# Performance work log

Hardware: AMD Instinct MI355X
Metric: run time of the kernel (lower is better)

The kernel has to match this reference:

```python
import jax, jax.numpy as jnp
import numpy as np

EPS_BN = 1e-5
EPS_LN = 1e-5
B_, CIN, COUT, H_, W_ = 8, 64, 128, 64, 64
DSTATE, DCONV, EXPAND = 16, 4, 2
DINNER = EXPAND * COUT            # 256
DTRANK = (COUT + 15) // 16        # 8


def setup_inputs() -> dict:
    key = jax.random.key(0)
    ks = jax.random.split(key, 24)
    g = lambda i, shape, s=0.02: jax.random.normal(ks[i], shape, jnp.float32) * s
    inp = {}
    inp["x"] = jax.random.normal(ks[0], (B_, CIN, H_, W_), jnp.float32)
    # conv-bn-relu x2
    inp["conv1_w"] = g(1, (COUT, CIN, 3, 3), 0.05)
    inp["conv1_b"] = jnp.zeros((COUT,), jnp.float32)
    inp["bn1_g"] = jnp.ones((COUT,), jnp.float32)
    inp["bn1_b"] = jnp.zeros((COUT,), jnp.float32)
    inp["bn1_m"] = g(2, (COUT,), 0.1)
    inp["bn1_v"] = jnp.ones((COUT,), jnp.float32)
    inp["conv2_w"] = g(3, (COUT, COUT, 3, 3), 0.05)
    inp["conv2_b"] = jnp.zeros((COUT,), jnp.float32)
    inp["bn2_g"] = jnp.ones((COUT,), jnp.float32)
    inp["bn2_b"] = jnp.zeros((COUT,), jnp.float32)
    inp["bn2_m"] = g(4, (COUT,), 0.1)
    inp["bn2_v"] = jnp.ones((COUT,), jnp.float32)
    # Mamba params (mamba_ssm defaults: projections bias-free except dt_proj)
    inp["in_proj_w"] = g(5, (2 * DINNER, COUT))
    inp["conv1d_w"] = g(6, (DINNER, 1, DCONV), 0.1)   # depthwise
    inp["conv1d_b"] = jnp.zeros((DINNER,), jnp.float32)
    inp["x_proj_w"] = g(7, (DTRANK + 2 * DSTATE, DINNER))
    inp["dt_proj_w"] = g(8, (DINNER, DTRANK), 0.1)
    inp["dt_proj_b"] = g(9, (DINNER,), 0.5)
    # S4D-real init: A = -[1..d_state] per channel
    A = jnp.tile(jnp.arange(1, DSTATE + 1, dtype=jnp.float32)[None, :], (DINNER, 1))
    inp["A_log"] = jnp.log(A)
    inp["D"] = jnp.ones((DINNER,), jnp.float32)
    inp["out_proj_w"] = g(10, (COUT, DINNER))
    inp["ln_g"] = jnp.ones((COUT,), jnp.float32)
    inp["ln_b"] = jnp.zeros((COUT,), jnp.float32)
    return inp


def _conv3x3(x, w, b):
    y = jax.lax.conv_general_dilated(x, w, (1, 1), ((1, 1), (1, 1)),
                                     dimension_numbers=("NCHW", "OIHW", "NCHW"))
    return y + b[None, :, None, None]


def _bn_eval(x, g, b, m, v):
    inv = jax.lax.rsqrt(v + EPS_BN)
    return (x - m[None, :, None, None]) * (g * inv)[None, :, None, None] + b[None, :, None, None]


def _mamba(x_flat, in_proj_w, conv1d_w, conv1d_b, x_proj_w, dt_proj_w, dt_proj_b, A_log, D, out_proj_w):
    # x_flat: (B, L, C)
    Bsz, L, _ = x_flat.shape
    xz = jnp.einsum("blc,ec->ble", x_flat, in_proj_w)          # (B, L, 2*di)
    xm, z = jnp.split(xz, 2, axis=-1)                           # each (B, L, di)
    # causal depthwise conv1d over time
    xt = jnp.transpose(xm, (0, 2, 1))                           # (B, di, L)
    xt = jax.lax.conv_general_dilated(xt, conv1d_w, (1,), ((DCONV - 1, 0),),
                                      dimension_numbers=("NCH", "OIH", "NCH"),
                                      feature_group_count=DINNER)
    xt = xt + conv1d_b[None, :, None]
    x_ssm = jax.nn.silu(jnp.transpose(xt, (0, 2, 1)))           # (B, L, di)
    xdb = jnp.einsum("bld,ed->ble", x_ssm, x_proj_w)            # (B, L, dt_rank+2*ds)
    dt_r = xdb[..., :DTRANK]
    Bm = xdb[..., DTRANK:DTRANK + DSTATE]                       # (B, L, ds)
    Cm = xdb[..., DTRANK + DSTATE:]                             # (B, L, ds)
    dt = jax.nn.softplus(jnp.einsum("blr,dr->bld", dt_r, dt_proj_w) + dt_proj_b)
    A = -jnp.exp(A_log)                                         # (di, ds)

    def step(h, inp):
        dt_t, B_t, C_t, x_t = inp                               # (B,di) (B,ds) (B,ds) (B,di)
        dA = jnp.exp(dt_t[:, :, None] * A)                      # (B, di, ds)
        h = dA * h + (dt_t * x_t)[:, :, None] * B_t[:, None, :]
        y = jnp.einsum("bds,bs->bd", h, C_t)
        return h, y

    xs = (jnp.swapaxes(dt, 0, 1), jnp.swapaxes(Bm, 0, 1),
          jnp.swapaxes(Cm, 0, 1), jnp.swapaxes(x_ssm, 0, 1))
    h0 = jnp.zeros((Bsz, DINNER, DSTATE), jnp.float32)
    _, ys = jax.lax.scan(step, h0, xs)                          # (L, B, di)
    y = jnp.swapaxes(ys, 0, 1) + D * x_ssm
    y = y * jax.nn.silu(z)
    return jnp.einsum("bld,od->blo", y, out_proj_w)             # (B, L, C)


def reference(x, conv1_w, conv1_b, bn1_g, bn1_b, bn1_m, bn1_v,
              conv2_w, conv2_b, bn2_g, bn2_b, bn2_m, bn2_v,
              in_proj_w, conv1d_w, conv1d_b, x_proj_w, dt_proj_w, dt_proj_b,
              A_log, D, out_proj_w, ln_g, ln_b):
    h = jax.nn.relu(_bn_eval(_conv3x3(x, conv1_w, conv1_b), bn1_g, bn1_b, bn1_m, bn1_v))
    h = jax.nn.relu(_bn_eval(_conv3x3(h, conv2_w, conv2_b), bn2_g, bn2_b, bn2_m, bn2_v))
    Bsz, C, Hh, Ww = h.shape
    seq = jnp.transpose(h, (0, 2, 3, 1)).reshape(Bsz, Hh * Ww, C)
    seq = _mamba(seq, in_proj_w, conv1d_w, conv1d_b, x_proj_w,
                 dt_proj_w, dt_proj_b, A_log, D, out_proj_w)
    # LayerNorm over channels
    mu = jnp.mean(seq, axis=-1, keepdims=True)
    var = jnp.mean(jnp.square(seq - mu), axis=-1, keepdims=True)
    seq = (seq - mu) * jax.lax.rsqrt(var + EPS_LN) * ln_g + ln_b
    return jnp.transpose(seq.reshape(Bsz, Hh, Ww, C), (0, 3, 1, 2))
```

## Files before the change

kernel.cpp:

```cpp
#include <hip/hip_runtime.h>
#include <hip/hip_bf16.h>


typedef __attribute__((ext_vector_type(8))) short bf16x8;
typedef __attribute__((ext_vector_type(4))) float f32x4;

#define DEV __device__ __forceinline__

constexpr float LOG2E = 1.44269504088896f;

DEV float siluf(float v) {
  return v * __builtin_amdgcn_rcpf(1.f + __expf(-v));
}

DEV unsigned short f2bf(float f) {
  __hip_bfloat16 h = __float2bfloat16(f);
  return *reinterpret_cast<unsigned short*>(&h);
}

DEV float bf2f(unsigned short u) {
  unsigned int x = (unsigned int)u << 16;
  return __builtin_bit_cast(float, x);
}

DEV void gll16(const void* g, void* l) {
  __builtin_amdgcn_global_load_lds(
      (const __attribute__((address_space(1))) void*)g,
      (__attribute__((address_space(3))) void*)l, 16, 0, 0);
}

constexpr int NC = 256;
constexpr int CL = 16;

__global__ __launch_bounds__(256) void nchw2nhwc_bf16(
    const float* __restrict__ X, unsigned short* __restrict__ Xb)
{
  __shared__ float t[64][65];
  const int by = blockIdx.x;
  const int b = by >> 6, y = by & 63;
  const int tid = threadIdx.x;
  for (int i = tid; i < 4096; i += 256) {
    int c = i >> 6, xx = i & 63;
    t[c][xx] = X[(((size_t)b * 64 + c) * 64 + y) * 64 + xx];
  }
  __syncthreads();
  for (int i = tid; i < 4096; i += 256) {
    int xx = i >> 6, c = i & 63;
    Xb[(((size_t)(b * 66 + y + 1) * 66) + xx + 1) * 64 + c] = f2bf(t[c][xx]);
  }
}

__global__ __launch_bounds__(256) void prep_all(
    const float* __restrict__ conv1_w, const float* __restrict__ conv2_w,
    const float* __restrict__ in_proj_w, const float* __restrict__ out_proj_w,
    const float* __restrict__ x_proj_w, const float* __restrict__ A_log,
    unsigned short* __restrict__ wb1, unsigned short* __restrict__ wb2,
    unsigned short* __restrict__ win, unsigned short* __restrict__ wout,
    unsigned short* __restrict__ xpwb, float* __restrict__ An2f)
{
  int idx = blockIdx.x * 256 + threadIdx.x;
  if (idx < 73728) {
    int co = idx / 576, r = idx % 576, t = r >> 6, ci = r & 63;
    wb1[idx] = f2bf(conv1_w[((size_t)co * 64 + ci) * 9 + t]);
  } else if (idx < 221184) {
    int i = idx - 73728;
    int co = i / 1152, r = i % 1152, t = r >> 7, ci = r & 127;
    wb2[i] = f2bf(conv2_w[((size_t)co * 128 + ci) * 9 + t]);
  } else if (idx < 286720) {
    int i = idx - 221184; win[i] = f2bf(in_proj_w[i]);
  } else if (idx < 319488) {
    int i = idx - 286720; wout[i] = f2bf(out_proj_w[i]);
  } else if (idx < 352256) {
    int i = idx - 319488; int r = i >> 8, c = i & 255;
    xpwb[i] = (r < 40) ? f2bf(x_proj_w[r * 256 + c]) : (unsigned short)0;
  } else if (idx < 356352) {
    int i = idx - 352256;
    An2f[i] = -__expf(A_log[i]) * LOG2E;
  }
}

template<int CI, int PADOUT>
__global__ __launch_bounds__(256) void conv_mfma(
    const unsigned short* __restrict__ Xp,
    const unsigned short* __restrict__ Wb,
    const float* __restrict__ bc,
    const float* __restrict__ bg, const float* __restrict__ bb,
    const float* __restrict__ bm, const float* __restrict__ bv,
    unsigned short* __restrict__ Y)
{
  constexpr int KC  = 3 * CI / 64;
  constexpr int NCH = 3 * KC;
  __shared__ bf16x8 ldsA[2][512];

  const int lane = threadIdx.x & 63;
  const int wid  = threadIdx.x >> 6;
  const int n0 = wid * 32;
  const int y = blockIdx.x, b = blockIdx.y;
  const int lr = lane & 15, kq = lane >> 4, lk = kq * 8;

  auto stage = [&](int buf, int c) {
    const int dy = c / KC, kc = c - dy * KC;
    const unsigned short* g = Xp
        + (size_t)((b * 66 + y + dy) * 66) * CI
        + (size_t)lane * CI + kc * 64 + wid * 16;
    gll16(g,     &ldsA[buf][(wid * 2) * 64]);
    gll16(g + 8, &ldsA[buf][(wid * 2 + 1) * 64]);
  };

  f32x4 acc[4][2];
  #pragma unroll
  for (int i = 0; i < 4; ++i)
    #pragma unroll
    for (int j = 0; j < 2; ++j) acc[i][j] = f32x4{0.f, 0.f, 0.f, 0.f};

  stage(0, 0);
  __syncthreads();

  #pragma unroll
  for (int c = 0; c < NCH; ++c) {
    if (c + 1 < NCH) stage((c + 1) & 1, c + 1);
    const int dy = c / KC, kc = c - dy * KC;
    bf16x8 bw[2][2];
    #pragma unroll
    for (int t = 0; t < 2; ++t)
      #pragma unroll
      for (int nf = 0; nf < 2; ++nf)
        bw[t][nf] = *reinterpret_cast<const bf16x8*>(
            Wb + (size_t)(n0 + nf * 16 + lr) * (9 * CI)
               + dy * 3 * CI + kc * 64 + t * 32 + lk);
    const bf16x8* Ab = ldsA[c & 1];
    #pragma unroll
    for (int t = 0; t < 2; ++t)
      #pragma unroll
      for (int mf = 0; mf < 4; ++mf) {
        bf16x8 afr = Ab[(t * 4 + kq) * 64 + mf * 16 + lr];
        #pragma unroll
        for (int nf = 0; nf < 2; ++nf)
          acc[mf][nf] = __builtin_amdgcn_mfma_f32_16x16x32_bf16(
              afr, bw[t][nf], acc[mf][nf], 0, 0, 0);
      }
    __syncthreads();
  }

  #pragma unroll
  for (int nf = 0; nf < 2; ++nf) {
    int n = n0 + nf * 16 + lr;
    float aS = bg[n] * rsqrtf(bv[n] + 1e-5f);
    float aB = (bc[n] - bm[n]) * aS + bb[n];
    #pragma unroll
    for (int mf = 0; mf < 4; ++mf)
      #pragma unroll
      for (int i = 0; i < 4; ++i) {
        int m = mf * 16 + kq * 4 + i;
        float v = fmaxf(acc[mf][nf][i] * aS + aB, 0.f);
        if (PADOUT)
          Y[((size_t)(b * 66 + y + 1) * 66 + m + 1) * 128 + n] = f2bf(v);
        else
          Y[((size_t)(b * 4096 + y * 64 + m)) * 128 + n] = f2bf(v);
      }
  }
}

template<int KDIM, int EPI>
__global__ __launch_bounds__(256) void gemm_mfma(
    const unsigned short* __restrict__ A,
    const unsigned short* __restrict__ Wn,
    float* __restrict__ C0,
    unsigned short* __restrict__ Cb0, unsigned short* __restrict__ Cb1)
{
  constexpr int NCH = KDIM / 64;
  __shared__ bf16x8 ldsA[2][512];

  const int lane = threadIdx.x & 63;
  const int wid  = threadIdx.x >> 6;
  const int m0 = blockIdx.x * 64;
  const int n0 = blockIdx.y * 128 + wid * 32;
  const int lr = lane & 15, kq = lane >> 4, lk = kq * 8;

  bf16x8 bw[NCH][2][2];
  #pragma unroll
  for (int c = 0; c < NCH; ++c)
    #pragma unroll
    for (int t = 0; t < 2; ++t)
      #pragma unroll
      for (int nf = 0; nf < 2; ++nf)
        bw[c][t][nf] = *reinterpret_cast<const bf16x8*>(
            Wn + (size_t)(n0 + nf * 16 + lr) * KDIM + c * 64 + t * 32 + lk);

  auto stage = [&](int buf, int c) {
    const unsigned short* g = A + (size_t)(m0 + lane) * KDIM + c * 64 + wid * 16;
    gll16(g,     &ldsA[buf][(wid * 2) * 64]);
    gll16(g + 8, &ldsA[buf][(wid * 2 + 1) * 64]);
  };

  f32x4 acc[4][2];
  #pragma unroll
  for (int i = 0; i < 4; ++i)
    #pragma unroll
    for (int j = 0; j < 2; ++j) acc[i][j] = f32x4{0.f, 0.f, 0.f, 0.f};

  stage(0, 0);
  __syncthreads();

  #pragma unroll
  for (int c = 0; c < NCH; ++c) {
    if (c + 1 < NCH) stage((c + 1) & 1, c + 1);
    const bf16x8* Ab = ldsA[c & 1];
    #pragma unroll
    for (int t = 0; t < 2; ++t)
      #pragma unroll
      for (int mf = 0; mf < 4; ++mf) {
        bf16x8 afr = Ab[(t * 4 + kq) * 64 + mf * 16 + lr];
        #pragma unroll
        for (int nf = 0; nf < 2; ++nf)
          acc[mf][nf] = __builtin_amdgcn_mfma_f32_16x16x32_bf16(
              afr, bw[c][t][nf], acc[mf][nf], 0, 0, 0);
      }
    __syncthreads();
  }

  #pragma unroll
  for (int nf = 0; nf < 2; ++nf) {
    int n = n0 + nf * 16 + lr;
    #pragma unroll
    for (int mf = 0; mf < 4; ++mf)
      #pragma unroll
      for (int i = 0; i < 4; ++i) {
        int m = m0 + mf * 16 + kq * 4 + i;
        float v = acc[mf][nf][i];
        if (EPI == 0) {
          if (n < 256) Cb0[(size_t)m * 256 + n] = f2bf(v);
          else         Cb1[(size_t)m * 256 + (n - 256)] = f2bf(v);
        } else if (EPI == 1) {
          C0[(size_t)m * 128 + n] = v;
        } else {
          if (n < 40) C0[(size_t)m * 40 + n] = v;
        }
      }
  }
}

__global__ __launch_bounds__(256) void conv1d_silu(
    const unsigned short* __restrict__ xm,
    const float* __restrict__ w,
    const float* __restrict__ bias,
    unsigned short* __restrict__ out)
{
  __shared__ float ws4[4][256];
  __shared__ float bsh[256];
  for (int i = threadIdx.x; i < 1024; i += 256)
    ws4[i >> 8][i & 255] = w[(i & 255) * 4 + (i >> 8)];
  bsh[threadIdx.x] = bias[threadIdx.x];
  __syncthreads();
  const int total = 32768 * 32;
  for (int idx = blockIdx.x * 256 + threadIdx.x; idx < total;
       idx += gridDim.x * 256) {
    int d8 = idx & 31, t = idx >> 5, l = t & 4095;
    int d = d8 * 8;
    float acc[8];
    #pragma unroll
    for (int k = 0; k < 8; ++k) acc[k] = bsh[d + k];
    #pragma unroll
    for (int j = 0; j < 4; ++j) {
      if (l - 3 + j >= 0) {
        uint4 xv = *reinterpret_cast<const uint4*>(
            &xm[(size_t)(t - 3 + j) * 256 + d]);
        const unsigned short* xs = reinterpret_cast<const unsigned short*>(&xv);
        #pragma unroll
        for (int k = 0; k < 8; ++k)
          acc[k] = fmaf(bf2f(xs[k]), ws4[j][d + k], acc[k]);
      }
    }
    unsigned int pk[4];
    #pragma unroll
    for (int k = 0; k < 4; ++k) {
      unsigned short lo = f2bf(siluf(acc[2 * k]));
      unsigned short hi = f2bf(siluf(acc[2 * k + 1]));
      pk[k] = (unsigned int)lo | ((unsigned int)hi << 16);
    }
    *reinterpret_cast<uint4*>(&out[(size_t)t * 256 + d]) =
        *reinterpret_cast<uint4*>(pk);
  }
}

__global__ __launch_bounds__(256) void scan_pass1(
    const unsigned short* __restrict__ xssm, const float* __restrict__ xdb,
    const float* __restrict__ dtw, const float* __restrict__ dtb,
    const float* __restrict__ An2f,
    unsigned short* __restrict__ Qb, float* __restrict__ S)
{
  __shared__ __align__(16) float sh[CL][40];
  const int c = blockIdx.x, b = blockIdx.y;
  const int d = threadIdx.x;
  if (threadIdx.x < CL * 10) {
    const float4* src = reinterpret_cast<const float4*>(
        &xdb[((size_t)b * 4096 + c * CL) * 40]);
    reinterpret_cast<float4*>(&sh[0][0])[threadIdx.x] = src[threadIdx.x];
  }
  float4 w0 = *reinterpret_cast<const float4*>(&dtw[d * 8]);
  float4 w1 = *reinterpret_cast<const float4*>(&dtw[d * 8 + 4]);
  const float bdt = dtb[d];
  float An2[16], h[16];
  {
    const f32x4* a2 = reinterpret_cast<const f32x4*>(&An2f[d * 16]);
    #pragma unroll
    for (int q = 0; q < 4; ++q) {
      f32x4 v = a2[q];
      An2[q * 4 + 0] = v[0]; An2[q * 4 + 1] = v[1];
      An2[q * 4 + 2] = v[2]; An2[q * 4 + 3] = v[3];
    }
  }
  #pragma unroll
  for (int s = 0; s < 16; ++s) h[s] = 0.f;
  __syncthreads();

  float sdt = 0.f;
  const size_t xbase = ((size_t)b * 4096 + (size_t)c * CL) * 256 + d;
  unsigned short xu = xssm[xbase];
  for (int l = 0; l < CL; ++l) {
    unsigned short xun = (l + 1 < CL) ? xssm[xbase + (size_t)(l + 1) * 256]
                                      : (unsigned short)0;
    const float4* row = reinterpret_cast<const float4*>(sh[l]);
    float4 r0 = row[0], r1 = row[1];
    float acc = bdt;
    acc = fmaf(r0.x, w0.x, acc); acc = fmaf(r0.y, w0.y, acc);
    acc = fmaf(r0.z, w0.z, acc); acc = fmaf(r0.w, w0.w, acc);
    acc = fmaf(r1.x, w1.x, acc); acc = fmaf(r1.y, w1.y, acc);
    acc = fmaf(r1.z, w1.z, acc); acc = fmaf(r1.w, w1.w, acc);
    float dt = (acc > 20.f) ? acc : __logf(1.f + __expf(acc));
    sdt += dt;
    float dtx = dt * bf2f(xu);
    #pragma unroll
    for (int q = 0; q < 4; ++q) {
      float4 Bq = row[2 + q];
      float bb4[4] = {Bq.x, Bq.y, Bq.z, Bq.w};
      #pragma unroll
      for (int j = 0; j < 4; ++j) {
        int s = q * 4 + j;
        float dA = __builtin_amdgcn_exp2f(dt * An2[s]);
        h[s] = fmaf(dA, h[s], dtx * bb4[j]);
      }
    }
    xu = xun;
  }
  unsigned int pk[8];
  #pragma unroll
  for (int k = 0; k < 8; ++k)
    pk[k] = (unsigned int)f2bf(h[2 * k]) | ((unsigned int)f2bf(h[2 * k + 1]) << 16);
  uint4* qp = reinterpret_cast<uint4*>(
      &Qb[(((size_t)b * NC + c) * 256 + d) * 16]);
  qp[0] = *reinterpret_cast<uint4*>(pk);
  qp[1] = *reinterpret_cast<uint4*>(pk + 4);
  S[((size_t)b * NC + c) * 256 + d] = sdt;
}

__global__ __launch_bounds__(256) void scan_combine(
    unsigned short* __restrict__ Qb, const float* __restrict__ S,
    const float* __restrict__ An2f)
{
  int g = blockIdx.x * 256 + threadIdx.x;
  int b = g >> 12, d = (g >> 4) & 255, s = g & 15;
  float An2 = An2f[d * 16 + s];
  const size_t qbase = (size_t)b * NC * 4096 + d * 16 + s;
  const size_t sbase = (size_t)b * NC * 256 + d;
  float h = 0.f;
  unsigned short qn = Qb[qbase];
  float sn = S[sbase];
  for (int c = 0; c < NC; ++c) {
    float q = bf2f(qn), sd = sn;
    if (c + 1 < NC) {
      qn = Qb[qbase + (size_t)(c + 1) * 4096];
      sn = S[sbase + (size_t)(c + 1) * 256];
    }
    Qb[qbase + (size_t)c * 4096] = f2bf(h);
    h = fmaf(__builtin_amdgcn_exp2f(An2 * sd), h, q);
  }
}

__global__ __launch_bounds__(256) void scan_pass2(
    const unsigned short* __restrict__ xssm, const float* __restrict__ xdb,
    const unsigned short* __restrict__ zb,
    const float* __restrict__ dtw, const float* __restrict__ dtb,
    const float* __restrict__ An2f, const float* __restrict__ Dp,
    const unsigned short* __restrict__ Hstart, unsigned short* __restrict__ ybf)
{
  __shared__ __align__(16) float sh[CL][40];
  const int c = blockIdx.x, b = blockIdx.y;
  const int d = threadIdx.x;
  if (threadIdx.x < CL * 10) {
    const float4* src = reinterpret_cast<const float4*>(
        &xdb[((size_t)b * 4096 + c * CL) * 40]);
    reinterpret_cast<float4*>(&sh[0][0])[threadIdx.x] = src[threadIdx.x];
  }
  float4 w0 = *reinterpret_cast<const float4*>(&dtw[d * 8]);
  float4 w1 = *reinterpret_cast<const float4*>(&dtw[d * 8 + 4]);
  const float bdt = dtb[d];
  const float Dd = Dp[d];
  float An2[16], h[16];
  {
    const f32x4* a2 = reinterpret_cast<const f32x4*>(&An2f[d * 16]);
    #pragma unroll
    for (int q = 0; q < 4; ++q) {
      f32x4 v = a2[q];
      An2[q * 4 + 0] = v[0]; An2[q * 4 + 1] = v[1];
      An2[q * 4 + 2] = v[2]; An2[q * 4 + 3] = v[3];
    }
  }
  {
    const uint4* hp = reinterpret_cast<const uint4*>(
        &Hstart[(((size_t)b * NC + c) * 256 + d) * 16]);
    uint4 h0 = hp[0], h1 = hp[1];
    const unsigned short* hs = reinterpret_cast<const unsigned short*>(&h0);
    #pragma unroll
    for (int s = 0; s < 8; ++s) h[s] = bf2f(hs[s]);
    const unsigned short* hs2 = reinterpret_cast<const unsigned short*>(&h1);
    #pragma unroll
    for (int s = 0; s < 8; ++s) h[8 + s] = bf2f(hs2[s]);
  }
  __syncthreads();

  const size_t xbase = ((size_t)b * 4096 + (size_t)c * CL) * 256 + d;
  unsigned short xu = xssm[xbase], zu = zb[xbase];
  for (int l = 0; l < CL; ++l) {
    unsigned short xun = 0, zun = 0;
    if (l + 1 < CL) {
      xun = xssm[xbase + (size_t)(l + 1) * 256];
      zun = zb[xbase + (size_t)(l + 1) * 256];
    }
    const float4* row = reinterpret_cast<const float4*>(sh[l]);
    float4 r0 = row[0], r1 = row[1];
    float acc = bdt;
    acc = fmaf(r0.x, w0.x, acc); acc = fmaf(r0.y, w0.y, acc);
    acc = fmaf(r0.z, w0.z, acc); acc = fmaf(r0.w, w0.w, acc);
    acc = fmaf(r1.x, w1.x, acc); acc = fmaf(r1.y, w1.y, acc);
    acc = fmaf(r1.z, w1.z, acc); acc = fmaf(r1.w, w1.w, acc);
    float dt = (acc > 20.f) ? acc : __logf(1.f + __expf(acc));
    float xv = bf2f(xu);
    float dtx = dt * xv;
    float yq[4] = {0.f, 0.f, 0.f, 0.f};
    #pragma unroll
    for (int q = 0; q < 4; ++q) {
      float4 Bq = row[2 + q], Cq = row[6 + q];
      float bb4[4] = {Bq.x, Bq.y, Bq.z, Bq.w};
      float cc4[4] = {Cq.x, Cq.y, Cq.z, Cq.w};
      #pragma unroll
      for (int j = 0; j < 4; ++j) {
        int s = q * 4 + j;
        float dA = __builtin_amdgcn_exp2f(dt * An2[s]);
        h[s] = fmaf(dA, h[s], dtx * bb4[j]);
        yq[q] = fmaf(h[s], cc4[j], yq[q]);
      }
    }
    float y = (yq[0] + yq[1]) + (yq[2] + yq[3]);
    y = (y + Dd * xv) * siluf(bf2f(zu));
    ybf[xbase + (size_t)l * 256] = f2bf(y);
    xu = xun; zu = zun;
  }
}

__global__ __launch_bounds__(256) void ln_transpose(
    const float* __restrict__ X,
    const float* __restrict__ g, const float* __restrict__ b,
    float* __restrict__ out)
{
  __shared__ float buf[64][129];
  const int t0 = blockIdx.x * 64;
  const int bb = t0 >> 12, l0 = t0 & 4095;
  const int tid = threadIdx.x;
  for (int idx = tid; idx < 64 * 128; idx += 256)
    buf[idx >> 7][idx & 127] = X[(size_t)t0 * 128 + idx];
  __syncthreads();
  const int tt = tid >> 2, q = tid & 3;
  float s = 0.f, sq = 0.f;
  #pragma unroll
  for (int i = 0; i < 32; ++i) {
    float v = buf[tt][q * 32 + i];
    s += v; sq += v * v;
  }
  s  += __shfl_xor(s, 1);  s  += __shfl_xor(s, 2);
  sq += __shfl_xor(sq, 1); sq += __shfl_xor(sq, 2);
  float mu = s * (1.f / 128.f);
  float var = sq * (1.f / 128.f) - mu * mu;
  float rstd = rsqrtf(fmaxf(var, 0.f) + 1e-5f);
  #pragma unroll
  for (int i = 0; i < 32; ++i) {
    int c = q * 32 + i;
    buf[tt][c] = (buf[tt][c] - mu) * rstd * g[c] + b[c];
  }
  __syncthreads();
  for (int idx = tid; idx < 64 * 128; idx += 256) {
    int c = idx >> 6, t2 = idx & 63;
    out[((size_t)bb * 128 + c) * 4096 + l0 + t2] = buf[t2][c];
  }
}

extern "C" void kernel_launch(void* const* d_in, const int* in_sizes, int n_in,
                              void* d_out, int out_size, void* d_ws, size_t ws_size,
                              hipStream_t stream) {
  const float* x        = (const float*)d_in[0];
  const float* conv1_w  = (const float*)d_in[1];
  const float* conv1_b  = (const float*)d_in[2];
  const float* bn1_g    = (const float*)d_in[3];
  const float* bn1_b    = (const float*)d_in[4];
  const float* bn1_m    = (const float*)d_in[5];
  const float* bn1_v    = (const float*)d_in[6];
  const float* conv2_w  = (const float*)d_in[7];
  const float* conv2_b  = (const float*)d_in[8];
  const float* bn2_g    = (const float*)d_in[9];
  const float* bn2_b    = (const float*)d_in[10];
  const float* bn2_m    = (const float*)d_in[11];
  const float* bn2_v    = (const float*)d_in[12];
  const float* in_proj_w  = (const float*)d_in[13];
  const float* conv1d_w   = (const float*)d_in[14];
  const float* conv1d_b   = (const float*)d_in[15];
  const float* x_proj_w   = (const float*)d_in[16];
  const float* dt_proj_w  = (const float*)d_in[17];
  const float* dt_proj_b  = (const float*)d_in[18];
  const float* A_log      = (const float*)d_in[19];
  const float* Dp         = (const float*)d_in[20];
  const float* out_proj_w = (const float*)d_in[21];
  const float* ln_g       = (const float*)d_in[22];
  const float* ln_b       = (const float*)d_in[23];
  float* out = (float*)d_out;

  float* ws_f = (float*)d_ws;
  unsigned short* xbp  = (unsigned short*)ws_f;
  unsigned short* xmb  = (unsigned short*)ws_f;
  unsigned short* ybf  = (unsigned short*)ws_f;
  float*          xdb  = ws_f + 4194304;
  float*          Sbuf = ws_f + 5505024;
  float*          outs = ws_f + 4194304;
  unsigned short* zbu  = (unsigned short*)(ws_f + 8388608);
  unsigned short* xsu  = (unsigned short*)(ws_f + 12582912);
  unsigned short* h1p  = (unsigned short*)(ws_f + 16777216);
  unsigned short* seqb = (unsigned short*)(ws_f + 19007488);
  unsigned short* Qb   = (unsigned short*)(ws_f + 16777216);
  unsigned short* wb1  = (unsigned short*)(ws_f + 25165824);
  unsigned short* wb2  = (unsigned short*)(ws_f + 25202688);
  unsigned short* win  = (unsigned short*)(ws_f + 25276416);
  unsigned short* wout = (unsigned short*)(ws_f + 25309184);
  unsigned short* xpwb = (unsigned short*)(ws_f + 25325568);
  float*          An2f = ws_f + 25341952;

  hipMemsetAsync(xbp, 0, (size_t)8 * 66 * 66 * 64 * 2, stream);
  hipMemsetAsync(h1p, 0, (size_t)8 * 66 * 66 * 128 * 2, stream);

  nchw2nhwc_bf16<<<512, 256, 0, stream>>>(x, xbp);
  prep_all<<<1392, 256, 0, stream>>>(conv1_w, conv2_w, in_proj_w, out_proj_w,
                                     x_proj_w, A_log,
                                     wb1, wb2, win, wout, xpwb, An2f);

  conv_mfma<64, 1><<<dim3(64, 8), 256, 0, stream>>>(
      xbp, wb1, conv1_b, bn1_g, bn1_b, bn1_m, bn1_v, h1p);
  conv_mfma<128, 0><<<dim3(64, 8), 256, 0, stream>>>(
      h1p, wb2, conv2_b, bn2_g, bn2_b, bn2_m, bn2_v, seqb);

  gemm_mfma<128, 0><<<dim3(512, 4), 256, 0, stream>>>(
      seqb, win, nullptr, xmb, zbu);

  conv1d_silu<<<2048, 256, 0, stream>>>(xmb, conv1d_w, conv1d_b, xsu);

  gemm_mfma<256, 2><<<dim3(512, 1), 256, 0, stream>>>(
      xsu, xpwb, xdb, nullptr, nullptr);

  scan_pass1<<<dim3(NC, 8), 256, 0, stream>>>(
      xsu, xdb, dt_proj_w, dt_proj_b, An2f, Qb, Sbuf);
  scan_combine<<<128, 256, 0, stream>>>(Qb, Sbuf, An2f);
  scan_pass2<<<dim3(NC, 8), 256, 0, stream>>>(
      xsu, xdb, zbu, dt_proj_w, dt_proj_b, An2f, Dp, Qb, ybf);

  gemm_mfma<256, 1><<<dim3(512, 1), 256, 0, stream>>>(
      ybf, wout, outs, nullptr, nullptr);
  ln_transpose<<<512, 256, 0, stream>>>(outs, ln_g, ln_b, out);
}
```

Measured before the change: 218.5 us.

## Fuse out-projection GEMM with LayerNorm and merge prologue kernels

The out_proj GEMM and the LayerNorm/transpose now run in one kernel: accumulators go straight into shared memory, are normalized, and are written out in NCHW, so the fp32 intermediate no longer makes a round trip through global memory. The input transpose, the weight preparation and the padding setup are merged into one prologue launch. That launch zeroes only the border rows and columns of the padded buffers, replacing two full-buffer memsets. Together this removes several launches and a large share of memory traffic; the cost is more LDS per block in the fused kernel (about 49KB) and correctness now depends on the border-zeroing logic.

Measured after the change: 207.2 us. 1.05x faster.

```diff
diff --git a/kernel.cpp b/kernel.cpp
--- a/kernel.cpp
+++ b/kernel.cpp
@@ -32,50 +32,65 @@
 constexpr int NC = 256;
 constexpr int CL = 16;
 
-__global__ __launch_bounds__(256) void nchw2nhwc_bf16(
-    const float* __restrict__ X, unsigned short* __restrict__ Xb)
-{
-  __shared__ float t[64][65];
-  const int by = blockIdx.x;
-  const int b = by >> 6, y = by & 63;
-  const int tid = threadIdx.x;
-  for (int i = tid; i < 4096; i += 256) {
-    int c = i >> 6, xx = i & 63;
-    t[c][xx] = X[(((size_t)b * 64 + c) * 64 + y) * 64 + xx];
-  }
-  __syncthreads();
-  for (int i = tid; i < 4096; i += 256) {
-    int xx = i >> 6, c = i & 63;
-    Xb[(((size_t)(b * 66 + y + 1) * 66) + xx + 1) * 64 + c] = f2bf(t[c][xx]);
-  }
-}
-
-__global__ __launch_bounds__(256) void prep_all(
+DEV void zero_border(unsigned short* buf, int CI, int tid0, int nthreads) {
+  for (int w = tid0; w < 8 * 260; w += nthreads) {
+    int b = w / 260, e = w % 260;
+    int y, x;
+    if (e < 132) { y = (e < 66) ? 0 : 65; x = (e < 66) ? e : e - 66; }
+    else { int e2 = e - 132; y = 1 + (e2 >> 1); x = (e2 & 1) ? 65 : 0; }
+    uint4* p = reinterpret_cast<uint4*>(buf + ((size_t)((b * 66 + y) * 66 + x)) * CI);
+    for (int k = 0; k < CI / 8; ++k) p[k] = uint4{0u, 0u, 0u, 0u};
+  }
+}
+
+__global__ __launch_bounds__(256) void prologue(
+    const float* __restrict__ X, unsigned short* __restrict__ Xb,
     const float* __restrict__ conv1_w, const float* __restrict__ conv2_w,
     const float* __restrict__ in_proj_w, const float* __restrict__ out_proj_w,
     const float* __restrict__ x_proj_w, const float* __restrict__ A_log,
     unsigned short* __restrict__ wb1, unsigned short* __restrict__ wb2,
     unsigned short* __restrict__ win, unsigned short* __restrict__ wout,
-    unsigned short* __restrict__ xpwb, float* __restrict__ An2f)
-{
-  int idx = blockIdx.x * 256 + threadIdx.x;
-  if (idx < 73728) {
-    int co = idx / 576, r = idx % 576, t = r >> 6, ci = r & 63;
-    wb1[idx] = f2bf(conv1_w[((size_t)co * 64 + ci) * 9 + t]);
-  } else if (idx < 221184) {
-    int i = idx - 73728;
-    int co = i / 1152, r = i % 1152, t = r >> 7, ci = r & 127;
-    wb2[i] = f2bf(conv2_w[((size_t)co * 128 + ci) * 9 + t]);
-  } else if (idx < 286720) {
-    int i = idx - 221184; win[i] = f2bf(in_proj_w[i]);
-  } else if (idx < 319488) {
-    int i = idx - 286720; wout[i] = f2bf(out_proj_w[i]);
-  } else if (idx < 352256) {
-    int i = idx - 319488; int r = i >> 8, c = i & 255;
-    xpwb[i] = (r < 40) ? f2bf(x_proj_w[r * 256 + c]) : (unsigned short)0;
-  } else if (idx < 356352) {
-    int i = idx - 352256;
-    An2f[i] = -__expf(A_log[i]) * LOG2E;
+    unsigned short* __restrict__ xpwb, float* __restrict__ An2f,
+    unsigned short* __restrict__ h1p)
+{
+  __shared__ float t[64][65];
+  const int blk = blockIdx.x;
+  const int tid = threadIdx.x;
+  if (blk < 512) {
+    const int b = blk >> 6, y = blk & 63;
+    for (int i = tid; i < 4096; i += 256) {
+      int c = i >> 6, xx = i & 63;
+      t[c][xx] = X[(((size_t)b * 64 + c) * 64 + y) * 64 + xx];
+    }
+    __syncthreads();
+    for (int i = tid; i < 4096; i += 256) {
+      int xx = i >> 6, c = i & 63;
+      Xb[(((size_t)(b * 66 + y + 1) * 66) + xx + 1) * 64 + c] = f2bf(t[c][xx]);
+    }
+  } else if (blk < 1904) {
+    int idx = (blk - 512) * 256 + tid;
+    if (idx < 73728) {
+      int co = idx / 576, r = idx % 576, tp = r >> 6, ci = r & 63;
+      wb1[idx] = f2bf(conv1_w[((size_t)co * 64 + ci) * 9 + tp]);
+    } else if (idx < 221184) {
+      int i = idx - 73728;
+      int co = i / 1152, r = i % 1152, tp = r >> 7, ci = r & 127;
+      wb2[i] = f2bf(conv2_w[((size_t)co * 128 + ci) * 9 + tp]);
+    } else if (idx < 286720) {
+      int i = idx - 221184; win[i] = f2bf(in_proj_w[i]);
+    } else if (idx < 319488) {
+      int i = idx - 286720; wout[i] = f2bf(out_proj_w[i]);
+    } else if (idx < 352256) {
+      int i = idx - 319488; int r = i >> 8, c = i & 255;
+      xpwb[i] = (r < 40) ? f2bf(x_proj_w[r * 256 + c]) : (unsigned short)0;
+    } else if (idx < 356352) {
+      int i = idx - 352256;
+      An2f[i] = -__expf(A_log[i]) * LOG2E;
+    }
+  } else {
+    int tid0 = (blk - 1904) * 256 + tid;
+    zero_border(Xb, 64, tid0, 16 * 256);
+    zero_border(h1p, 128, tid0, 16 * 256);
   }
 }
 
@@ -231,12 +246,107 @@
         if (EPI == 0) {
           if (n < 256) Cb0[(size_t)m * 256 + n] = f2bf(v);
           else         Cb1[(size_t)m * 256 + (n - 256)] = f2bf(v);
-        } else if (EPI == 1) {
-          C0[(size_t)m * 128 + n] = v;
         } else {
           if (n < 40) C0[(size_t)m * 40 + n] = v;
         }
       }
+  }
+}
+
+__global__ __launch_bounds__(256) void outproj_ln(
+    const unsigned short* __restrict__ A,
+    const unsigned short* __restrict__ Wn,
+    const float* __restrict__ lg, const float* __restrict__ lb,
+    float* __restrict__ out)
+{
+  constexpr int KDIM = 256;
+  constexpr int NCH = KDIM / 64;
+  __shared__ bf16x8 ldsA[2][512];
+  __shared__ float buf[64][129];
+
+  const int lane = threadIdx.x & 63;
+  const int wid  = threadIdx.x >> 6;
+  const int m0 = blockIdx.x * 64;
+  const int n0 = wid * 32;
+  const int lr = lane & 15, kq = lane >> 4, lk = kq * 8;
+
+  bf16x8 bw[NCH][2][2];
+  #pragma unroll
+  for (int c = 0; c < NCH; ++c)
+    #pragma unroll
+    for (int t = 0; t < 2; ++t)
+      #pragma unroll
+      for (int nf = 0; nf < 2; ++nf)
+        bw[c][t][nf] = *reinterpret_cast<const bf16x8*>(
+            Wn + (size_t)(n0 + nf * 16 + lr) * KDIM + c * 64 + t * 32 + lk);
+
+  auto stage = [&](int buf2, int c) {
+    const unsigned short* g = A + (size_t)(m0 + lane) * KDIM + c * 64 + wid * 16;
+    gll16(g,     &ldsA[buf2][(wid * 2) * 64]);
+    gll16(g + 8, &ldsA[buf2][(wid * 2 + 1) * 64]);
+  };
+
+  f32x4 acc[4][2];
+  #pragma unroll
+  for (int i = 0; i < 4; ++i)
+    #pragma unroll
+    for (int j = 0; j < 2; ++j) acc[i][j] = f32x4{0.f, 0.f, 0.f, 0.f};
+
+  stage(0, 0);
+  __syncthreads();
+
+  #pragma unroll
+  for (int c = 0; c < NCH; ++c) {
+    if (c + 1 < NCH) stage((c + 1) & 1, c + 1);
+    const bf16x8* Ab = ldsA[c & 1];
+    #pragma unroll
+    for (int t = 0; t < 2; ++t)
+      #pragma unroll
+      for (int mf = 0; mf < 4; ++mf) {
+        bf16x8 afr = Ab[(t * 4 + kq) * 64 + mf * 16 + lr];
+        #pragma unroll
+        for (int nf = 0; nf < 2; ++nf)
+          acc[mf][nf] = __builtin_amdgcn_mfma_f32_16x16x32_bf16(
+              afr, bw[c][t][nf], acc[mf][nf], 0, 0, 0);
+      }
+    __syncthreads();
+  }
+
+  #pragma unroll
+  for (int nf = 0; nf < 2; ++nf) {
+    int n = n0 + nf * 16 + lr;
+    #pragma unroll
+    for (int mf = 0; mf < 4; ++mf)
+      #pragma unroll
+      for (int i = 0; i < 4; ++i)
+        buf[mf * 16 + kq * 4 + i][n] = acc[mf][nf][i];
+  }
+  __syncthreads();
+
+  const int tid = threadIdx.x;
+  const int tt = tid >> 2, q = tid & 3;
+  float s = 0.f, sq = 0.f;
+  #pragma unroll
+  for (int i = 0; i < 32; ++i) {
+    float v = buf[tt][q * 32 + i];
+    s += v; sq += v * v;
+  }
+  s  += __shfl_xor(s, 1);  s  += __shfl_xor(s, 2);
+  sq += __shfl_xor(sq, 1); sq += __shfl_xor(sq, 2);
+  float mu = s * (1.f / 128.f);
+  float var = sq * (1.f / 128.f) - mu * mu;
+  float rstd = rsqrtf(fmaxf(var, 0.f) + 1e-5f);
+  #pragma unroll
+  for (int i = 0; i < 32; ++i) {
+    int c = q * 32 + i;
+    buf[tt][c] = (buf[tt][c] - mu) * rstd * lg[c] + lb[c];
+  }
+  __syncthreads();
+
+  const int bb = m0 >> 12, l0 = m0 & 4095;
+  for (int idx = tid; idx < 64 * 128; idx += 256) {
+    int c = idx >> 6, t2 = idx & 63;
+    out[((size_t)bb * 128 + c) * 4096 + l0 + t2] = buf[t2][c];
   }
 }
 
@@ -455,42 +565,6 @@
     y = (y + Dd * xv) * siluf(bf2f(zu));
     ybf[xbase + (size_t)l * 256] = f2bf(y);
     xu = xun; zu = zun;
-  }
-}
-
-__global__ __launch_bounds__(256) void ln_transpose(
-    const float* __restrict__ X,
-    const float* __restrict__ g, const float* __restrict__ b,
-    float* __restrict__ out)
-{
-  __shared__ float buf[64][129];
-  const int t0 = blockIdx.x * 64;
-  const int bb = t0 >> 12, l0 = t0 & 4095;
-  const int tid = threadIdx.x;
-  for (int idx = tid; idx < 64 * 128; idx += 256)
-    buf[idx >> 7][idx & 127] = X[(size_t)t0 * 128 + idx];
-  __syncthreads();
-  const int tt = tid >> 2, q = tid & 3;
-  float s = 0.f, sq = 0.f;
-  #pragma unroll
-  for (int i = 0; i < 32; ++i) {
-    float v = buf[tt][q * 32 + i];
-    s += v; sq += v * v;
-  }
-  s  += __shfl_xor(s, 1);  s  += __shfl_xor(s, 2);
-  sq += __shfl_xor(sq, 1); sq += __shfl_xor(sq, 2);
-  float mu = s * (1.f / 128.f);
-  float var = sq * (1.f / 128.f) - mu * mu;
-  float rstd = rsqrtf(fmaxf(var, 0.f) + 1e-5f);
-  #pragma unroll
-  for (int i = 0; i < 32; ++i) {
-    int c = q * 32 + i;
-    buf[tt][c] = (buf[tt][c] - mu) * rstd * g[c] + b[c];
-  }
-  __syncthreads();
-  for (int idx = tid; idx < 64 * 128; idx += 256) {
-    int c = idx >> 6, t2 = idx & 63;
-    out[((size_t)bb * 128 + c) * 4096 + l0 + t2] = buf[t2][c];
   }
 }
 
@@ -529,7 +603,6 @@
   unsigned short* ybf  = (unsigned short*)ws_f;
   float*          xdb  = ws_f + 4194304;
   float*          Sbuf = ws_f + 5505024;
-  float*          outs = ws_f + 4194304;
   unsigned short* zbu  = (unsigned short*)(ws_f + 8388608);
   unsigned short* xsu  = (unsigned short*)(ws_f + 12582912);
   unsigned short* h1p  = (unsigned short*)(ws_f + 16777216);
@@ -542,13 +615,9 @@
   unsigned short* xpwb = (unsigned short*)(ws_f + 25325568);
   float*          An2f = ws_f + 25341952;
 
-  hipMemsetAsync(xbp, 0, (size_t)8 * 66 * 66 * 64 * 2, stream);
-  hipMemsetAsync(h1p, 0, (size_t)8 * 66 * 66 * 128 * 2, stream);
-
-  nchw2nhwc_bf16<<<512, 256, 0, stream>>>(x, xbp);
-  prep_all<<<1392, 256, 0, stream>>>(conv1_w, conv2_w, in_proj_w, out_proj_w,
-                                     x_proj_w, A_log,
-                                     wb1, wb2, win, wout, xpwb, An2f);
+  prologue<<<1920, 256, 0, stream>>>(
+      x, xbp, conv1_w, conv2_w, in_proj_w, out_proj_w, x_proj_w, A_log,
+      wb1, wb2, win, wout, xpwb, An2f, h1p);
 
   conv_mfma<64, 1><<<dim3(64, 8), 256, 0, stream>>>(
       xbp, wb1, conv1_b, bn1_g, bn1_b, bn1_m, bn1_v, h1p);
@@ -569,7 +638,5 @@
   scan_pass2<<<dim3(NC, 8), 256, 0, stream>>>(
       xsu, xdb, zbu, dt_proj_w, dt_proj_b, An2f, Dp, Qb, ybf);
 
-  gemm_mfma<256, 1><<<dim3(512, 1), 256, 0, stream>>>(
-      ybf, wout, outs, nullptr, nullptr);
-  ln_transpose<<<512, 256, 0, stream>>>(outs, ln_g, ln_b, out);
-}
+  outproj_ln<<<512, 256, 0, stream>>>(ybf, wout, ln_g, ln_b, out);
+}
```
